# Kernel tuning notes

Hardware: AMD Instinct MI355X
Metric: run time of the kernel (lower is better)

The kernel has to match this reference:

```python
import jax, jax.numpy as jnp
import numpy as np

C_IN = 128
DIM = 2 * C_IN          # ELAN final channels = 2*in_channels = 256
WS = 8                  # window size
HEADS = 8
HEAD_DIM = DIM // HEADS
B, H, W = 4, 128, 128
LN_EPS = 1e-5


def setup_inputs() -> dict:
    key = jax.random.key(0)
    ks = jax.random.split(key, 20)
    mid = C_IN // 2  # middle_channels == block_channels == 64

    def p(k, shape, scale=0.05):
        return jax.random.normal(k, shape, jnp.float32) * scale

    return dict(
        x=jax.random.normal(ks[0], (B, C_IN, H, W), jnp.float32),
        # ELAN stem 1x1 convs: [main, short], each folded BN (scale, bias)
        w_stem=p(ks[1], (2, mid, C_IN, 1, 1)),
        s_stem=1.0 + p(ks[2], (2, mid)),
        b_stem=p(ks[3], (2, mid)),
        # 2 blocks x 2 convs of 3x3, mid->mid
        w_blk=p(ks[4], (4, mid, mid, 3, 3)),
        s_blk=1.0 + p(ks[5], (4, mid)),
        b_blk=p(ks[6], (4, mid)),
        # SwinV2 block params
        norm1_g=jnp.ones((DIM,), jnp.float32),
        norm1_b=jnp.zeros((DIM,), jnp.float32),
        qkv_w=p(ks[7], (3 * DIM, DIM)),
        qkv_b=p(ks[8], (3 * DIM,)).at[DIM:2 * DIM].set(0.0),  # V2 zeroes k bias
        proj_w=p(ks[9], (DIM, DIM)),
        proj_b=p(ks[10], (DIM,)),
        logit_scale=jnp.full((HEADS, 1, 1), float(np.log(10.0)), jnp.float32),
        cpb_w1=p(ks[11], (512, 2)),
        cpb_b1=p(ks[12], (512,)),
        cpb_w2=p(ks[13], (HEADS, 512)),
        norm2_g=jnp.ones((DIM,), jnp.float32),
        norm2_b=jnp.zeros((DIM,), jnp.float32),
        mlp_w1=p(ks[14], (DIM, DIM)),  # mlp_ratio=1.0
        mlp_b1=p(ks[15], (DIM,)),
        mlp_w2=p(ks[16], (DIM, DIM)),
        mlp_b2=p(ks[17], (DIM,)),
    )


def convbn(x, w, s, b, pad):
    # Conv(no bias) + eval-mode BN folded into per-channel scale/bias + SiLU
    y = jax.lax.conv_general_dilated(
        x, w, (1, 1), [(pad, pad), (pad, pad)],
        dimension_numbers=("NCHW", "OIHW", "NCHW"))
    y = y * s[None, :, None, None] + b[None, :, None, None]
    return jax.nn.silu(y)


def layernorm(x, g, b):
    m = jnp.mean(x, -1, keepdims=True)
    v = jnp.var(x, -1, keepdims=True)
    return (x - m) * jax.lax.rsqrt(v + LN_EPS) * g + b


def _rel_bias_consts():
    ws = WS
    ch = np.arange(-(ws - 1), ws, dtype=np.float32)
    table = np.stack(np.meshgrid(ch, ch, indexing="ij"), axis=-1)  # [2ws-1,2ws-1,2]
    table = table / (ws - 1) * 8.0
    table = np.sign(table) * np.log2(np.abs(table) + 1.0) / 3.0
    coords = np.stack(np.meshgrid(np.arange(ws), np.arange(ws), indexing="ij")).reshape(2, -1)
    rel = (coords[:, :, None] - coords[:, None, :]).transpose(1, 2, 0)  # [N,N,2]
    rel[..., 0] += ws - 1
    rel[..., 1] += ws - 1
    rel[..., 0] *= 2 * ws - 1
    idx = rel.sum(-1).reshape(-1)
    return jnp.asarray(table.reshape(-1, 2)), jnp.asarray(idx)


_TABLE, _IDX = _rel_bias_consts()


def elan_swin(x, w_stem, s_stem, b_stem, w_blk, s_blk, b_blk, norm1_g, norm1_b,
              qkv_w, qkv_b, proj_w, proj_b, logit_scale, cpb_w1, cpb_b1, cpb_w2,
              norm2_g, norm2_b, mlp_w1, mlp_b1, mlp_w2, mlp_b2):
    # ---- ELANBlock ----
    x_short = convbn(x, w_stem[1], s_stem[1], b_stem[1], 0)
    x_main = convbn(x, w_stem[0], s_stem[0], b_stem[0], 0)
    xb = x_main
    outs = []
    for i in range(2):
        xb = convbn(xb, w_blk[2 * i], s_blk[2 * i], b_blk[2 * i], 1)
        xb = convbn(xb, w_blk[2 * i + 1], s_blk[2 * i + 1], b_blk[2 * i + 1], 1)
        outs.append(xb)
    e = jnp.concatenate([outs[1], outs[0], x_main, x_short], axis=1)  # [B,DIM,H,W]
    e = e.transpose(0, 2, 3, 1)  # NHWC

    # ---- ShiftedWindowAttentionV2 (shift=0, H,W divisible by WS) ----
    Bn, Hh, Ww, Cc = e.shape
    nH, nW = Hh // WS, Ww // WS
    N = WS * WS
    xw = e.reshape(Bn, nH, WS, nW, WS, Cc).transpose(0, 1, 3, 2, 4, 5).reshape(-1, N, Cc)
    qkv = xw @ qkv_w.T + qkv_b
    qkv = qkv.reshape(-1, N, 3, HEADS, HEAD_DIM).transpose(2, 0, 3, 1, 4)
    q, k, v = qkv[0], qkv[1], qkv[2]  # [Bw, heads, N, d]
    qn = q / jnp.maximum(jnp.linalg.norm(q, axis=-1, keepdims=True), 1e-12)
    kn = k / jnp.maximum(jnp.linalg.norm(k, axis=-1, keepdims=True), 1e-12)
    attn = jnp.einsum("whnd,whmd->whnm", qn, kn)
    scale = jnp.exp(jnp.minimum(logit_scale, jnp.log(100.0)))  # [heads,1,1]
    attn = attn * scale[None]
    # continuous position bias MLP
    bias = jax.nn.relu(_TABLE @ cpb_w1.T + cpb_b1) @ cpb_w2.T  # [(2ws-1)^2, heads]
    bias = bias[_IDX].reshape(N, N, HEADS).transpose(2, 0, 1)
    bias = 16.0 * jax.nn.sigmoid(bias)
    attn = jax.nn.softmax(attn + bias[None], axis=-1)
    out = jnp.einsum("whnm,whmd->whnd", attn, v).transpose(0, 2, 1, 3).reshape(-1, N, Cc)
    out = out @ proj_w.T + proj_b
    out = out.reshape(Bn, nH, nW, WS, WS, Cc).transpose(0, 1, 3, 2, 4, 5).reshape(Bn, Hh, Ww, Cc)

    # ---- SwinTransformerBlockV2 (post-norm residuals) ----
    s = e + layernorm(out, norm1_g, norm1_b)
    h = s @ mlp_w1.T + mlp_b1
    h = jax.nn.gelu(h, approximate=False)
    h = h @ mlp_w2.T + mlp_b2
    s = s + layernorm(h, norm2_g, norm2_b)
    return s.transpose(0, 3, 1, 2)  # NCHW


def reference(x, w_stem, s_stem, b_stem, w_blk, s_blk, b_blk, norm1_g, norm1_b,
              qkv_w, qkv_b, proj_w, proj_b, logit_scale, cpb_w1, cpb_b1, cpb_w2,
              norm2_g, norm2_b, mlp_w1, mlp_b1, mlp_w2, mlp_b2):
    return elan_swin(x, w_stem, s_stem, b_stem, w_blk, s_blk, b_blk, norm1_g, norm1_b,
                     qkv_w, qkv_b, proj_w, proj_b, logit_scale, cpb_w1, cpb_b1, cpb_w2,
                     norm2_g, norm2_b, mlp_w1, mlp_b1, mlp_w2, mlp_b2)
```

## Files before the change

kernel.cpp:

```cpp
#include <hip/hip_runtime.h>
#include <hip/hip_bf16.h>
#include <math.h>


#define HW 16384
typedef unsigned int u32;
typedef unsigned short u16;
typedef __attribute__((ext_vector_type(8))) short short8;
typedef __attribute__((ext_vector_type(4))) float floatx4;

__device__ __forceinline__ float silu_f(float y) { return y / (1.f + expf(-y)); }
__device__ __forceinline__ float bflo(u32 u) { return __uint_as_float(u << 16); }
__device__ __forceinline__ float bfhi(u32 u) { return __uint_as_float(u & 0xffff0000u); }
__device__ __forceinline__ float bf2f(u16 v) { return __uint_as_float((u32)v << 16); }
__device__ __forceinline__ u16 f2bf(float x) {
  u32 u = __float_as_uint(x);
  u += 0x7fffu + ((u >> 16) & 1u);
  return (u16)(u >> 16);
}
__device__ __forceinline__ u32 pack2(float a, float b) {
  return (u32)f2bf(a) | ((u32)f2bf(b) << 16);
}

#define GLDS16(gp, lp)                                           \
  __builtin_amdgcn_global_load_lds(                              \
      (const __attribute__((address_space(1))) void*)(gp),       \
      (__attribute__((address_space(3))) void*)(lp), 16, 0, 0)

__global__ __launch_bounds__(256) void repack_kernel(
    const float* __restrict__ w_blk, const float* __restrict__ s_blk,
    const float* __restrict__ w_stem, const float* __restrict__ s_stem,
    u16* __restrict__ wtc, u16* __restrict__ wts) {
  int idx = blockIdx.x * 256 + threadIdx.x;
  if (idx < 147456) {
    int c = idx & 63;
    int rest = idx >> 6;
    int oc = rest & 63;
    int ct = rest >> 6;
    int conv = ct / 9, t = ct % 9;
    float w = w_blk[((size_t)(conv * 64 + oc) * 64 + c) * 9 + t];
    wtc[idx] = f2bf(w * s_blk[conv * 64 + oc]);
  } else if (idx < 147456 + 16384) {
    int j = idx - 147456;
    int c = j & 127, oc = j >> 7;
    float w = w_stem[(size_t)oc * 128 + c];
    wts[j] = f2bf(w * s_stem[oc]);
  }
}

__global__ __launch_bounds__(256) void castw_kernel(
    const float* __restrict__ in, u16* __restrict__ outp, int n) {
  int i = blockIdx.x * 256 + threadIdx.x;
  if (i < n) outp[i] = f2bf(in[i]);
}

__global__ __launch_bounds__(512) void cpb_mlp_kernel(
    const float* __restrict__ w1, const float* __restrict__ b1,
    const float* __restrict__ w2, float* __restrict__ pre) {
  __shared__ float hb[512];
  int t = blockIdx.x, j = threadIdx.x;
  int i = t / 15, jj = t % 15;
  float c0 = (float)(i - 7) * (8.f / 7.f);
  float c1 = (float)(jj - 7) * (8.f / 7.f);
  float s0 = (c0 > 0.f) ? 1.f : ((c0 < 0.f) ? -1.f : 0.f);
  float s1 = (c1 > 0.f) ? 1.f : ((c1 < 0.f) ? -1.f : 0.f);
  float t0 = s0 * log2f(fabsf(c0) + 1.f) * (1.f / 3.f);
  float t1 = s1 * log2f(fabsf(c1) + 1.f) * (1.f / 3.f);
  float h = t0 * w1[j * 2] + t1 * w1[j * 2 + 1] + b1[j];
  hb[j] = fmaxf(h, 0.f);
  __syncthreads();
  if (j < 8) {
    float s = 0.f;
    for (int k = 0; k < 512; ++k) s += hb[k] * w2[j * 512 + k];
    pre[t * 8 + j] = s;
  }
}

__global__ __launch_bounds__(256) void cpb_expand_kernel(
    const float* __restrict__ pre, float* __restrict__ bias_t) {
  int idx = blockIdx.x * 256 + threadIdx.x;
  int m = idx >> 6, n = idx & 63;
  int di = (n >> 3) - (m >> 3) + 7;
  int dj = (n & 7) - (m & 7) + 7;
  int ti = di * 15 + dj;
#pragma unroll
  for (int h = 0; h < 8; ++h) {
    float v = pre[ti * 8 + h];
    bias_t[h * 4096 + idx] = 16.f / (1.f + expf(-v));
  }
}

__global__ __launch_bounds__(256) void transpose_in_kernel(
    const float* __restrict__ x, u16* __restrict__ xt) {
  __shared__ float tl[64][65];
  int bid = blockIdx.x;
  int b = bid >> 9;
  int r = bid & 511;
  int cs = r >> 8, hws = r & 255;
  int c0 = cs << 6, hw0 = hws << 6;
  int tid = threadIdx.x;
  for (int e = tid; e < 4096; e += 256) {
    int c = e >> 6, p = e & 63;
    tl[c][p] = x[(size_t)(b * 128 + c0 + c) * HW + hw0 + p];
  }
  __syncthreads();
  for (int e = tid; e < 4096; e += 256) {
    int p = e >> 6, c = e & 63;
    xt[(size_t)(b * HW + hw0 + p) * 128 + c0 + c] = f2bf(tl[c][p]);
  }
}

__global__ __launch_bounds__(256, 4) void gemm_bf16_kernel(
    const u16* __restrict__ A, const u16* __restrict__ W,
    const float* __restrict__ bias, u16* __restrict__ C, int K, int ldc,
    int act) {
  __shared__ u16 As[128 * 64];
  __shared__ u16 Ws[64 * 64];
  int tid = threadIdx.x;
  int wv = tid >> 6, lane = tid & 63;
  int m0 = blockIdx.x * 128, n0 = blockIdx.y * 64;
  floatx4 zz = {0.f, 0.f, 0.f, 0.f};
  floatx4 acc[2][4];
#pragma unroll
  for (int i = 0; i < 2; ++i)
#pragma unroll
    for (int j = 0; j < 4; ++j) acc[i][j] = zz;
  int lr = lane >> 3, ls = lane & 7;
  for (int k0 = 0; k0 < K; k0 += 64) {
#pragma unroll
    for (int i = 0; i < 4; ++i) {
      int ci = wv * 4 + i;
      int r = ci * 8 + lr;
      int cc = ls ^ (r & 7);
      GLDS16(A + (size_t)(m0 + r) * K + k0 + cc * 8, As + ci * 512);
    }
#pragma unroll
    for (int i = 0; i < 2; ++i) {
      int ci = wv * 2 + i;
      int r = ci * 8 + lr;
      int cc = ls ^ (r & 7);
      GLDS16(W + (size_t)(n0 + r) * K + k0 + cc * 8, Ws + ci * 512);
    }
    __syncthreads();
#pragma unroll
    for (int kk = 0; kk < 2; ++kk) {
      int g = kk * 4 + (lane >> 4);
      short8 a0, a1, b0, b1, b2, b3;
      {
        int row = wv * 32 + (lane & 15);
        a0 = *(const short8*)&As[row * 64 + (g ^ (row & 7)) * 8];
        int row2 = row + 16;
        a1 = *(const short8*)&As[row2 * 64 + (g ^ (row2 & 7)) * 8];
      }
      {
        int col = lane & 15;
        b0 = *(const short8*)&Ws[col * 64 + (g ^ (col & 7)) * 8];
        int c1 = col + 16;
        b1 = *(const short8*)&Ws[c1 * 64 + (g ^ (c1 & 7)) * 8];
        int c2 = col + 32;
        b2 = *(const short8*)&Ws[c2 * 64 + (g ^ (c2 & 7)) * 8];
        int c3 = col + 48;
        b3 = *(const short8*)&Ws[c3 * 64 + (g ^ (c3 & 7)) * 8];
      }
      acc[0][0] = __builtin_amdgcn_mfma_f32_16x16x32_bf16(a0, b0, acc[0][0], 0, 0, 0);
      acc[0][1] = __builtin_amdgcn_mfma_f32_16x16x32_bf16(a0, b1, acc[0][1], 0, 0, 0);
      acc[0][2] = __builtin_amdgcn_mfma_f32_16x16x32_bf16(a0, b2, acc[0][2], 0, 0, 0);
      acc[0][3] = __builtin_amdgcn_mfma_f32_16x16x32_bf16(a0, b3, acc[0][3], 0, 0, 0);
      acc[1][0] = __builtin_amdgcn_mfma_f32_16x16x32_bf16(a1, b0, acc[1][0], 0, 0, 0);
      acc[1][1] = __builtin_amdgcn_mfma_f32_16x16x32_bf16(a1, b1, acc[1][1], 0, 0, 0);
      acc[1][2] = __builtin_amdgcn_mfma_f32_16x16x32_bf16(a1, b2, acc[1][2], 0, 0, 0);
      acc[1][3] = __builtin_amdgcn_mfma_f32_16x16x32_bf16(a1, b3, acc[1][3], 0, 0, 0);
    }
    __syncthreads();
  }
  int rbase = wv * 32 + ((lane >> 4) << 2);
  int cb = lane & 15;
#pragma unroll
  for (int mi = 0; mi < 2; ++mi) {
#pragma unroll
    for (int nj = 0; nj < 4; ++nj) {
      int col = n0 + nj * 16 + cb;
      float bv = bias[col];
#pragma unroll
      for (int r = 0; r < 4; ++r) {
        int row = m0 + rbase + mi * 16 + r;
        float v = acc[mi][nj][r] + bv;
        if (act == 1) v = 0.5f * v * (1.f + erff(v * 0.70710678118654752f));
        else if (act == 2) v = silu_f(v);
        C[(size_t)row * ldc + col] = f2bf(v);
      }
    }
  }
}

__global__ __launch_bounds__(256) void conv3x3_mfma_kernel(
    const u16* __restrict__ in, int istr, u16* __restrict__ outp, int ostr,
    const u16* __restrict__ wt, const float* __restrict__ bias) {
  __shared__ u16 tile[6400];
  int tid = threadIdx.x;
  int wv = tid >> 6, lane = tid & 63;
  int bx = blockIdx.x, by = blockIdx.y, b = blockIdx.z;
  int h0 = by * 8, w0 = bx * 8;
#pragma unroll
  for (int rr = 0; rr < 4; ++rr) {
    int slot = rr * 256 + tid;
    int p = slot >> 3, ch = slot & 7;
    if (p < 100) {
      int hr = p / 10, hc = p % 10;
      int gh = h0 + hr - 1, gw = w0 + hc - 1;
      bool ok = (gh >= 0) && (gh < 128) && (gw >= 0) && (gw < 128);
      uint4 v = {0u, 0u, 0u, 0u};
      if (ok) {
        size_t pix = (size_t)((b * 128 + gh) * 128 + gw);
        v = *(const uint4*)(in + pix * istr + ch * 8);
      }
      *(uint4*)(tile + p * 64 + ((ch ^ (p & 7)) << 3)) = v;
    }
  }
  __syncthreads();
  int pl = lane & 15;
  int g = lane >> 4;
  int prow = 2 * wv + (pl >> 3), pcol = pl & 7;
  floatx4 zz = {0.f, 0.f, 0.f, 0.f};
  floatx4 acc[4] = {zz, zz, zz, zz};
#pragma unroll
  for (int t = 0; t < 9; ++t) {
    int dy = t / 3, dx = t % 3;
    int hp = (prow + dy) * 10 + (pcol + dx);
    short8 bf0 = *(const short8*)&tile[hp * 64 + (((0 * 4 + g) ^ (hp & 7)) << 3)];
    short8 bf1 = *(const short8*)&tile[hp * 64 + (((1 * 4 + g) ^ (hp & 7)) << 3)];
    const u16* wtap = wt + t * 4096;
#pragma unroll
    for (int nf = 0; nf < 4; ++nf) {
      short8 a0 = *(const short8*)&wtap[(nf * 16 + pl) * 64 + g * 8];
      short8 a1 = *(const short8*)&wtap[(nf * 16 + pl) * 64 + 32 + g * 8];
      acc[nf] = __builtin_amdgcn_mfma_f32_16x16x32_bf16(a0, bf0, acc[nf], 0, 0, 0);
      acc[nf] = __builtin_amdgcn_mfma_f32_16x16x32_bf16(a1, bf1, acc[nf], 0, 0, 0);
    }
  }
  size_t pix = (size_t)((b * 128 + h0 + prow) * 128 + w0 + pcol);
#pragma unroll
  for (int nf = 0; nf < 4; ++nf) {
    float o0 = silu_f(acc[nf][0] + bias[nf * 16 + g * 4 + 0]);
    float o1 = silu_f(acc[nf][1] + bias[nf * 16 + g * 4 + 1]);
    float o2 = silu_f(acc[nf][2] + bias[nf * 16 + g * 4 + 2]);
    float o3 = silu_f(acc[nf][3] + bias[nf * 16 + g * 4 + 3]);
    uint2 w2;
    w2.x = pack2(o0, o1);
    w2.y = pack2(o2, o3);
    *(uint2*)(outp + pix * ostr + nf * 16 + g * 4) = w2;
  }
}

__global__ __launch_bounds__(256) void attn_mfma_kernel(
    const u16* __restrict__ qkv, const float* __restrict__ logit_scale,
    const float* __restrict__ bias_t, u16* __restrict__ ao) {
  __shared__ __align__(16) char lds[4 * 10240 + 4 * 4608];
  int tid = threadIdx.x;
  int w = tid >> 6, l = tid & 63;
  int wid = blockIdx.x >> 1;
  int h = __builtin_amdgcn_readfirstlane(((blockIdx.x & 1) << 2) + w);
  char* Aq = lds + w * 10240;
  char* Ak = Aq + 5120;
  char* Pt = Aq;
  char* Vt = lds + 40960 + w * 4608;
  char* Ol = Vt;

  int b = wid >> 8, wh = (wid >> 4) & 15, ww = wid & 15;
  int p = (b << 14) + ((wh * 8 + (l >> 3)) << 7) + ww * 8 + (l & 7);
  const u32* qp = (const u32*)(qkv + (size_t)p * 768 + h * 32);
  float scale = __expf(fminf(logit_scale[h], 4.6051701860f));
  int lc = l & 15, lg = l >> 4;

  {
    float f[32];
    float s = 0.f;
#pragma unroll
    for (int i = 0; i < 16; ++i) {
      u32 u = qp[i];
      f[2 * i] = bflo(u);
      f[2 * i + 1] = bfhi(u);
    }
#pragma unroll
    for (int d = 0; d < 32; ++d) s += f[d] * f[d];
    float r = scale / fmaxf(sqrtf(s), 1e-12f);
    uint4* dst = (uint4*)(Aq + l * 80);
#pragma unroll
    for (int c = 0; c < 4; ++c) {
      uint4 v;
      v.x = pack2(f[c * 8 + 0] * r, f[c * 8 + 1] * r);
      v.y = pack2(f[c * 8 + 2] * r, f[c * 8 + 3] * r);
      v.z = pack2(f[c * 8 + 4] * r, f[c * 8 + 5] * r);
      v.w = pack2(f[c * 8 + 6] * r, f[c * 8 + 7] * r);
      dst[c] = v;
    }
  }
  {
    float f[32];
    float s = 0.f;
#pragma unroll
    for (int i = 0; i < 16; ++i) {
      u32 u = qp[128 + i];
      f[2 * i] = bflo(u);
      f[2 * i + 1] = bfhi(u);
    }
#pragma unroll
    for (int d = 0; d < 32; ++d) s += f[d] * f[d];
    float r = 1.f / fmaxf(sqrtf(s), 1e-12f);
    uint4* dst = (uint4*)(Ak + l * 80);
#pragma unroll
    for (int c = 0; c < 4; ++c) {
      uint4 v;
      v.x = pack2(f[c * 8 + 0] * r, f[c * 8 + 1] * r);
      v.y = pack2(f[c * 8 + 2] * r, f[c * 8 + 3] * r);
      v.z = pack2(f[c * 8 + 4] * r, f[c * 8 + 5] * r);
      v.w = pack2(f[c * 8 + 6] * r, f[c * 8 + 7] * r);
      dst[c] = v;
    }
  }
  {
#pragma unroll
    for (int i = 0; i < 16; ++i) {
      u32 u = qp[256 + i];
      *(u16*)(Vt + (2 * i) * 144 + l * 2) = (u16)(u & 0xffffu);
      *(u16*)(Vt + (2 * i + 1) * 144 + l * 2) = (u16)(u >> 16);
    }
  }

  short8 kf[4], qf[4];
#pragma unroll
  for (int i = 0; i < 4; ++i) {
    kf[i] = *(const short8*)(Ak + (i * 16 + lc) * 80 + (lg << 4));
    qf[i] = *(const short8*)(Aq + (i * 16 + lc) * 80 + (lg << 4));
  }
  floatx4 zz = {0.f, 0.f, 0.f, 0.f};
  floatx4 S[4][4];
#pragma unroll
  for (int mi = 0; mi < 4; ++mi)
#pragma unroll
    for (int ni = 0; ni < 4; ++ni) S[mi][ni] = zz;
#pragma unroll
  for (int mi = 0; mi < 4; ++mi)
#pragma unroll
    for (int ni = 0; ni < 4; ++ni)
      S[mi][ni] = __builtin_amdgcn_mfma_f32_16x16x32_bf16(kf[mi], qf[ni], S[mi][ni], 0, 0, 0);

  const float* bh = bias_t + h * 4096;
  float den[4] = {0.f, 0.f, 0.f, 0.f};
#pragma unroll
  for (int mi = 0; mi < 4; ++mi) {
    int mb = mi * 16 + (lg << 2);
#pragma unroll
    for (int ni = 0; ni < 4; ++ni) {
      int nn = ni * 16 + lc;
#pragma unroll
      for (int r = 0; r < 4; ++r) {
        float e = __expf(S[mi][ni][r] + bh[(mb + r) * 64 + nn]);
        S[mi][ni][r] = e;
        den[ni] += e;
      }
    }
  }
#pragma unroll
  for (int ni = 0; ni < 4; ++ni) {
    den[ni] += __shfl_xor(den[ni], 16);
    den[ni] += __shfl_xor(den[ni], 32);
    den[ni] = 1.f / den[ni];
  }

#pragma unroll
  for (int ni = 0; ni < 4; ++ni)
#pragma unroll
    for (int mi = 0; mi < 4; ++mi) {
      uint2 v;
      v.x = pack2(S[mi][ni][0] * den[ni], S[mi][ni][1] * den[ni]);
      v.y = pack2(S[mi][ni][2] * den[ni], S[mi][ni][3] * den[ni]);
      *(uint2*)(Pt + (ni * 16 + lc) * 144 + mi * 32 + (lg << 3)) = v;
    }

  short8 vf[2][2];
#pragma unroll
  for (int ks = 0; ks < 2; ++ks)
#pragma unroll
    for (int db = 0; db < 2; ++db)
      vf[ks][db] = *(const short8*)(Vt + (db * 16 + lc) * 144 + ks * 64 + (lg << 4));
  floatx4 O[4][2];
#pragma unroll
  for (int nb = 0; nb < 4; ++nb) {
    O[nb][0] = zz;
    O[nb][1] = zz;
  }
#pragma unroll
  for (int nb = 0; nb < 4; ++nb) {
    short8 pf0 = *(const short8*)(Pt + (nb * 16 + lc) * 144 + (lg << 4));
    short8 pf1 = *(const short8*)(Pt + (nb * 16 + lc) * 144 + 64 + (lg << 4));
    O[nb][0] = __builtin_amdgcn_mfma_f32_16x16x32_bf16(pf0, vf[0][0], O[nb][0], 0, 0, 0);
    O[nb][0] = __builtin_amdgcn_mfma_f32_16x16x32_bf16(pf1, vf[1][0], O[nb][0], 0, 0, 0);
    O[nb][1] = __builtin_amdgcn_mfma_f32_16x16x32_bf16(pf0, vf[0][1], O[nb][1], 0, 0, 0);
    O[nb][1] = __builtin_amdgcn_mfma_f32_16x16x32_bf16(pf1, vf[1][1], O[nb][1], 0, 0, 0);
  }

#pragma unroll
  for (int nb = 0; nb < 4; ++nb)
#pragma unroll
    for (int r = 0; r < 4; ++r) {
      int n = nb * 16 + (lg << 2) + r;
      *(u16*)(Ol + n * 72 + lc * 2) = f2bf(O[nb][0][r]);
      *(u16*)(Ol + n * 72 + (16 + lc) * 2) = f2bf(O[nb][1][r]);
    }
  u32 ov[16];
#pragma unroll
  for (int j = 0; j < 16; ++j) ov[j] = *(const u32*)(Ol + l * 72 + j * 4);
  uint4* op = (uint4*)(ao + (size_t)(wid * 64 + l) * 256 + h * 32);
#pragma unroll
  for (int q4 = 0; q4 < 4; ++q4) {
    uint4 v;
    v.x = ov[q4 * 4 + 0];
    v.y = ov[q4 * 4 + 1];
    v.z = ov[q4 * 4 + 2];
    v.w = ov[q4 * 4 + 3];
    op[q4] = v;
  }
}

__global__ __launch_bounds__(256) void ln1v_kernel(
    const u16* __restrict__ pin, const u16* __restrict__ ebf,
    u16* __restrict__ sbf, const float* __restrict__ g,
    const float* __restrict__ bb) {
  int tid = threadIdx.x;
  int bid = blockIdx.x;
  int b = bid >> 8, hw0 = (bid & 255) << 6;
  int i = tid >> 2, qq = tid & 3;
  int hw = hw0 + i;
  int him = hw >> 7, wim = hw & 127;
  int wid = b * 256 + (him >> 3) * 16 + (wim >> 3);
  int t = wid * 64 + (him & 7) * 8 + (wim & 7);
  size_t pbase = (size_t)t * 256 + qq * 64;
  size_t ebase = ((size_t)(b * HW + hw)) * 256 + qq * 64;
  float v[64];
  float s1 = 0.f, s2 = 0.f;
#pragma unroll
  for (int j = 0; j < 8; ++j) {
    uint4 u = *(const uint4*)(pin + pbase + j * 8);
    u32 ua[4] = {u.x, u.y, u.z, u.w};
#pragma unroll
    for (int k = 0; k < 4; ++k) {
      float a = bflo(ua[k]), c = bfhi(ua[k]);
      v[j * 8 + 2 * k] = a;
      v[j * 8 + 2 * k + 1] = c;
      s1 += a + c;
      s2 += a * a + c * c;
    }
  }
  s1 += __shfl_xor(s1, 1);
  s1 += __shfl_xor(s1, 2);
  s2 += __shfl_xor(s2, 1);
  s2 += __shfl_xor(s2, 2);
  float mean = s1 * (1.f / 256.f);
  float var = s2 * (1.f / 256.f) - mean * mean;
  float rs = rsqrtf(var + 1e-5f);
#pragma unroll
  for (int j = 0; j < 8; ++j) {
    uint4 u = *(const uint4*)(ebf + ebase + j * 8);
    u32 ua[4] = {u.x, u.y, u.z, u.w};
    uint4 o;
    u32 ow[4];
#pragma unroll
    for (int k = 0; k < 4; ++k) {
      int c = qq * 64 + j * 8 + 2 * k;
      float o0 = bflo(ua[k]) + (v[j * 8 + 2 * k] - mean) * rs * g[c] + bb[c];
      float o1 = bfhi(ua[k]) + (v[j * 8 + 2 * k + 1] - mean) * rs * g[c + 1] + bb[c + 1];
      ow[k] = pack2(o0, o1);
    }
    o.x = ow[0]; o.y = ow[1]; o.z = ow[2]; o.w = ow[3];
    *(uint4*)(sbf + ebase + j * 8) = o;
  }
}

__global__ __launch_bounds__(256) void ln2t_kernel(
    const u16* __restrict__ h2, const u16* __restrict__ sbf,
    const float* __restrict__ g, const float* __restrict__ bb,
    float* __restrict__ outp) {
  __shared__ float tile[64][257];
  int tid = threadIdx.x;
  int bid = blockIdx.x;
  int b = bid >> 8, hw0 = (bid & 255) << 6;
  int i = tid >> 2, qq = tid & 3;
  size_t base = ((size_t)(b * HW + hw0 + i)) * 256 + qq * 64;
  float v[64];
  float s1 = 0.f, s2 = 0.f;
#pragma unroll
  for (int j = 0; j < 8; ++j) {
    uint4 u = *(const uint4*)(h2 + base + j * 8);
    u32 ua[4] = {u.x, u.y, u.z, u.w};
#pragma unroll
    for (int k = 0; k < 4; ++k) {
      float a = bflo(ua[k]), c = bfhi(ua[k]);
      v[j * 8 + 2 * k] = a;
      v[j * 8 + 2 * k + 1] = c;
      s1 += a + c;
      s2 += a * a + c * c;
    }
  }
  s1 += __shfl_xor(s1, 1);
  s1 += __shfl_xor(s1, 2);
  s2 += __shfl_xor(s2, 1);
  s2 += __shfl_xor(s2, 2);
  float mean = s1 * (1.f / 256.f);
  float var = s2 * (1.f / 256.f) - mean * mean;
  float rs = rsqrtf(var + 1e-5f);
#pragma unroll
  for (int j = 0; j < 8; ++j) {
    uint4 u = *(const uint4*)(sbf + base + j * 8);
    u32 ua[4] = {u.x, u.y, u.z, u.w};
#pragma unroll
    for (int k = 0; k < 4; ++k) {
      int c = qq * 64 + j * 8 + 2 * k;
      tile[i][c] = bflo(ua[k]) + (v[j * 8 + 2 * k] - mean) * rs * g[c] + bb[c];
      tile[i][c + 1] = bfhi(ua[k]) + (v[j * 8 + 2 * k + 1] - mean) * rs * g[c + 1] + bb[c + 1];
    }
  }
  __syncthreads();
  int pl = tid & 63, cq = tid >> 6;
#pragma unroll 8
  for (int cc = 0; cc < 64; ++cc) {
    int c = cq * 64 + cc;
    outp[((size_t)(b * 256 + c)) * HW + hw0 + pl] = tile[pl][c];
  }
}

extern "C" void kernel_launch(void* const* d_in, const int* in_sizes, int n_in,
                              void* d_out, int out_size, void* d_ws, size_t ws_size,
                              hipStream_t stream) {
  const float* x        = (const float*)d_in[0];
  const float* w_stem   = (const float*)d_in[1];
  const float* s_stem   = (const float*)d_in[2];
  const float* b_stem   = (const float*)d_in[3];
  const float* w_blk    = (const float*)d_in[4];
  const float* s_blk    = (const float*)d_in[5];
  const float* b_blk    = (const float*)d_in[6];
  const float* norm1_g  = (const float*)d_in[7];
  const float* norm1_b  = (const float*)d_in[8];
  const float* qkv_w    = (const float*)d_in[9];
  const float* qkv_b    = (const float*)d_in[10];
  const float* proj_w   = (const float*)d_in[11];
  const float* proj_b   = (const float*)d_in[12];
  const float* logit_sc = (const float*)d_in[13];
  const float* cpb_w1   = (const float*)d_in[14];
  const float* cpb_b1   = (const float*)d_in[15];
  const float* cpb_w2   = (const float*)d_in[16];
  const float* norm2_g  = (const float*)d_in[17];
  const float* norm2_b  = (const float*)d_in[18];
  const float* mlp_w1   = (const float*)d_in[19];
  const float* mlp_b1   = (const float*)d_in[20];
  const float* mlp_w2   = (const float*)d_in[21];
  const float* mlp_b2   = (const float*)d_in[22];
  float* out = (float*)d_out;
  float* ws = (float*)d_ws;
  (void)in_sizes; (void)n_in; (void)out_size; (void)ws_size;

  float* R0 = ws;
  float* R1 = ws + 16777216;
  float* R2 = ws + 33554432;
  float* TAIL = ws + 50331648;
  u16* WTC  = (u16*)TAIL;
  u16* WTS  = (u16*)(TAIL + 73728);
  u16* QWB  = (u16*)(TAIL + 81920);
  u16* PWB  = (u16*)(TAIL + 180224);
  u16* M1WB = (u16*)(TAIL + 212992);
  u16* M2WB = (u16*)(TAIL + 245760);
  float* BPRE = TAIL + 278528;
  float* BFT  = TAIL + 280576;

  u16* XT  = (u16*)R2;
  u16* EBF = (u16*)(R2 + 8388608);
  u16* T1  = (u16*)R1;
  u16* T2  = (u16*)(R1 + 2097152);
  u16* QKV = (u16*)R1;
  u16* AO  = (u16*)R0;
  u16* P   = (u16*)(R0 + 8388608);
  u16* SBF = (u16*)R0;
  u16* Hb  = (u16*)R2;
  u16* H2  = (u16*)(R0 + 8388608);

  repack_kernel<<<640, 256, 0, stream>>>(w_blk, s_blk, w_stem, s_stem, WTC, WTS);
  castw_kernel<<<768, 256, 0, stream>>>(qkv_w, QWB, 196608);
  castw_kernel<<<256, 256, 0, stream>>>(proj_w, PWB, 65536);
  castw_kernel<<<256, 256, 0, stream>>>(mlp_w1, M1WB, 65536);
  castw_kernel<<<256, 256, 0, stream>>>(mlp_w2, M2WB, 65536);
  cpb_mlp_kernel<<<225, 512, 0, stream>>>(cpb_w1, cpb_b1, cpb_w2, BPRE);
  cpb_expand_kernel<<<16, 256, 0, stream>>>(BPRE, BFT);

  transpose_in_kernel<<<2048, 256, 0, stream>>>(x, XT);
  dim3 gs(512, 2);
  gemm_bf16_kernel<<<gs, 256, 0, stream>>>(XT, WTS, b_stem, EBF + 128, 128, 256, 2);

  dim3 cgrid(16, 16, 4);
  conv3x3_mfma_kernel<<<cgrid, 256, 0, stream>>>(EBF + 128, 256, T1, 64, WTC, b_blk);
  conv3x3_mfma_kernel<<<cgrid, 256, 0, stream>>>(T1, 64, EBF + 64, 256, WTC + 9 * 4096, b_blk + 64);
  conv3x3_mfma_kernel<<<cgrid, 256, 0, stream>>>(EBF + 64, 256, T2, 64, WTC + 18 * 4096, b_blk + 128);
  conv3x3_mfma_kernel<<<cgrid, 256, 0, stream>>>(T2, 64, EBF, 256, WTC + 27 * 4096, b_blk + 192);

  dim3 gq(512, 12);
  gemm_bf16_kernel<<<gq, 256, 0, stream>>>(EBF, QWB, qkv_b, QKV, 256, 768, 0);

  attn_mfma_kernel<<<2048, 256, 0, stream>>>(QKV, logit_sc, BFT, AO);

  dim3 g4(512, 4);
  gemm_bf16_kernel<<<g4, 256, 0, stream>>>(AO, PWB, proj_b, P, 256, 256, 0);
  ln1v_kernel<<<1024, 256, 0, stream>>>(P, EBF, SBF, norm1_g, norm1_b);
  gemm_bf16_kernel<<<g4, 256, 0, stream>>>(SBF, M1WB, mlp_b1, Hb, 256, 256, 1);
  gemm_bf16_kernel<<<g4, 256, 0, stream>>>(Hb, M2WB, mlp_b2, H2, 256, 256, 0);
  ln2t_kernel<<<1024, 256, 0, stream>>>(H2, SBF, norm2_g, norm2_b, out);
}
```

Measured before the change: 464.3 us.

## Fuse QKV projection into window attention kernel with split-bf16 QK products

Removes the separate QKV GEMM and its 768-channel intermediate buffer. Each attention block now loads the 64-pixel window of the embedding into LDS and computes its four heads' Q, K and V with MFMA, reading the weights straight from global memory. The normalized Q and K are split into hi and lo bf16 parts, and the attention scores use three MFMAs for extra precision. Costs include redundant weight reads per block, triple MFMA work for the scores, and higher LDS use (72KB per block), which may lower occupancy.

```diff
diff --git a/kernel.cpp b/kernel.cpp
--- a/kernel.cpp
+++ b/kernel.cpp
@@ -8,6 +8,8 @@
 typedef unsigned short u16;
 typedef __attribute__((ext_vector_type(8))) short short8;
 typedef __attribute__((ext_vector_type(4))) float floatx4;
+
+#define MEMBAR() asm volatile("" ::: "memory")
 
 __device__ __forceinline__ float silu_f(float y) { return y / (1.f + expf(-y)); }
 __device__ __forceinline__ float bflo(u32 u) { return __uint_as_float(u << 16); }
@@ -252,98 +254,175 @@
   }
 }
 
-__global__ __launch_bounds__(256) void attn_mfma_kernel(
-    const u16* __restrict__ qkv, const float* __restrict__ logit_scale,
+__device__ __forceinline__ void qkv_mm(const u16* Elds, const u16* qwb,
+                                       int moff, int h, int lc, int lg,
+                                       floatx4 acc[4][2]) {
+  floatx4 zz = {0.f, 0.f, 0.f, 0.f};
+#pragma unroll
+  for (int mf = 0; mf < 4; ++mf) {
+    acc[mf][0] = zz;
+    acc[mf][1] = zz;
+  }
+#pragma unroll
+  for (int ks = 0; ks < 8; ++ks) {
+    int ch = ks >> 1, g = ((ks & 1) << 2) + lg;
+    short8 af[4];
+#pragma unroll
+    for (int mf = 0; mf < 4; ++mf) {
+      int tk = mf * 16 + lc;
+      af[mf] = *(const short8*)&Elds[(ch * 64 + tk) * 64 + ((g ^ (tk & 7)) << 3)];
+    }
+#pragma unroll
+    for (int nf = 0; nf < 2; ++nf) {
+      short8 bf = *(const short8*)(qwb +
+          (size_t)(moff + h * 32 + nf * 16 + lc) * 256 + ks * 32 + lg * 8);
+#pragma unroll
+      for (int mf = 0; mf < 4; ++mf)
+        acc[mf][nf] =
+            __builtin_amdgcn_mfma_f32_16x16x32_bf16(af[mf], bf, acc[mf][nf], 0, 0, 0);
+    }
+  }
+}
+
+__global__ __launch_bounds__(256) void attn_fused_kernel(
+    const u16* __restrict__ ebf, const u16* __restrict__ qwb,
+    const float* __restrict__ qkv_b, const float* __restrict__ logit_scale,
     const float* __restrict__ bias_t, u16* __restrict__ ao) {
-  __shared__ __align__(16) char lds[4 * 10240 + 4 * 4608];
+  __shared__ __align__(16) char lds[73728];
   int tid = threadIdx.x;
   int w = tid >> 6, l = tid & 63;
   int wid = blockIdx.x >> 1;
   int h = __builtin_amdgcn_readfirstlane(((blockIdx.x & 1) << 2) + w);
-  char* Aq = lds + w * 10240;
-  char* Ak = Aq + 5120;
-  char* Pt = Aq;
-  char* Vt = lds + 40960 + w * 4608;
+  u16* Elds = (u16*)lds;
+  char* Kn = lds + 32768 + w * 10240;
+  char* Qn = Kn + 5120;
+  char* Pt = Kn;
+  char* Vt = lds + w * 4608;
   char* Ol = Vt;
 
   int b = wid >> 8, wh = (wid >> 4) & 15, ww = wid & 15;
-  int p = (b << 14) + ((wh * 8 + (l >> 3)) << 7) + ww * 8 + (l & 7);
-  const u32* qp = (const u32*)(qkv + (size_t)p * 768 + h * 32);
+  int pixbase = (b << 14) + wh * 1024 + ww * 8;
+  {
+    int lr = l >> 3, ls = l & 7;
+#pragma unroll
+    for (int j = 0; j < 8; ++j) {
+      int pix = pixbase + j * 128 + lr;
+      GLDS16(ebf + (size_t)pix * 256 + w * 64 + ((ls ^ lr) << 3),
+             Elds + (w * 8 + j) * 512);
+    }
+  }
+  __syncthreads();
+
+  int lc = l & 15, lg = l >> 4;
   float scale = __expf(fminf(logit_scale[h], 4.6051701860f));
-  int lc = l & 15, lg = l >> 4;
-
+  floatx4 macc[4][2];
+  float rnrm[4][4];
+  short8 kf_hi[4], kf_lo[4], qf_hi[4], qf_lo[4];
+
+  qkv_mm(Elds, qwb, 256, h, lc, lg, macc);
+#pragma unroll
+  for (int mf = 0; mf < 4; ++mf)
+#pragma unroll
+    for (int r = 0; r < 4; ++r) {
+      float v0 = macc[mf][0][r], v1 = macc[mf][1][r];
+      float ss = v0 * v0 + v1 * v1;
+      ss += __shfl_xor(ss, 1);
+      ss += __shfl_xor(ss, 2);
+      ss += __shfl_xor(ss, 4);
+      ss += __shfl_xor(ss, 8);
+      float rk = 1.f / fmaxf(sqrtf(ss), 1e-12f);
+      rnrm[mf][r] = rk;
+      int tk = mf * 16 + (lg << 2) + r;
+      *(u16*)(Kn + tk * 80 + lc * 2) = f2bf(v0 * rk);
+      *(u16*)(Kn + tk * 80 + (16 + lc) * 2) = f2bf(v1 * rk);
+    }
+  MEMBAR();
+#pragma unroll
+  for (int i = 0; i < 4; ++i)
+    kf_hi[i] = *(const short8*)(Kn + (i * 16 + lc) * 80 + (lg << 4));
+  MEMBAR();
+#pragma unroll
+  for (int mf = 0; mf < 4; ++mf)
+#pragma unroll
+    for (int r = 0; r < 4; ++r) {
+      int tk = mf * 16 + (lg << 2) + r;
+      float s0 = macc[mf][0][r] * rnrm[mf][r];
+      float s1 = macc[mf][1][r] * rnrm[mf][r];
+      *(u16*)(Kn + tk * 80 + lc * 2) = f2bf(s0 - bf2f(f2bf(s0)));
+      *(u16*)(Kn + tk * 80 + (16 + lc) * 2) = f2bf(s1 - bf2f(f2bf(s1)));
+    }
+  MEMBAR();
+#pragma unroll
+  for (int i = 0; i < 4; ++i)
+    kf_lo[i] = *(const short8*)(Kn + (i * 16 + lc) * 80 + (lg << 4));
+  MEMBAR();
+
+  qkv_mm(Elds, qwb, 0, h, lc, lg, macc);
   {
-    float f[32];
-    float s = 0.f;
-#pragma unroll
-    for (int i = 0; i < 16; ++i) {
-      u32 u = qp[i];
-      f[2 * i] = bflo(u);
-      f[2 * i + 1] = bfhi(u);
-    }
-#pragma unroll
-    for (int d = 0; d < 32; ++d) s += f[d] * f[d];
-    float r = scale / fmaxf(sqrtf(s), 1e-12f);
-    uint4* dst = (uint4*)(Aq + l * 80);
-#pragma unroll
-    for (int c = 0; c < 4; ++c) {
-      uint4 v;
-      v.x = pack2(f[c * 8 + 0] * r, f[c * 8 + 1] * r);
-      v.y = pack2(f[c * 8 + 2] * r, f[c * 8 + 3] * r);
-      v.z = pack2(f[c * 8 + 4] * r, f[c * 8 + 5] * r);
-      v.w = pack2(f[c * 8 + 6] * r, f[c * 8 + 7] * r);
-      dst[c] = v;
-    }
-  }
-  {
-    float f[32];
-    float s = 0.f;
-#pragma unroll
-    for (int i = 0; i < 16; ++i) {
-      u32 u = qp[128 + i];
-      f[2 * i] = bflo(u);
-      f[2 * i + 1] = bfhi(u);
-    }
-#pragma unroll
-    for (int d = 0; d < 32; ++d) s += f[d] * f[d];
-    float r = 1.f / fmaxf(sqrtf(s), 1e-12f);
-    uint4* dst = (uint4*)(Ak + l * 80);
-#pragma unroll
-    for (int c = 0; c < 4; ++c) {
-      uint4 v;
-      v.x = pack2(f[c * 8 + 0] * r, f[c * 8 + 1] * r);
-      v.y = pack2(f[c * 8 + 2] * r, f[c * 8 + 3] * r);
-      v.z = pack2(f[c * 8 + 4] * r, f[c * 8 + 5] * r);
-      v.w = pack2(f[c * 8 + 6] * r, f[c * 8 + 7] * r);
-      dst[c] = v;
-    }
-  }
-  {
-#pragma unroll
-    for (int i = 0; i < 16; ++i) {
-      u32 u = qp[256 + i];
-      *(u16*)(Vt + (2 * i) * 144 + l * 2) = (u16)(u & 0xffffu);
-      *(u16*)(Vt + (2 * i + 1) * 144 + l * 2) = (u16)(u >> 16);
-    }
-  }
-
-  short8 kf[4], qf[4];
-#pragma unroll
-  for (int i = 0; i < 4; ++i) {
-    kf[i] = *(const short8*)(Ak + (i * 16 + lc) * 80 + (lg << 4));
-    qf[i] = *(const short8*)(Aq + (i * 16 + lc) * 80 + (lg << 4));
-  }
+    float qb0 = qkv_b[h * 32 + lc], qb1 = qkv_b[h * 32 + 16 + lc];
+#pragma unroll
+    for (int mf = 0; mf < 4; ++mf)
+#pragma unroll
+      for (int r = 0; r < 4; ++r) {
+        float v0 = macc[mf][0][r] + qb0, v1 = macc[mf][1][r] + qb1;
+        macc[mf][0][r] = v0;
+        macc[mf][1][r] = v1;
+        float ss = v0 * v0 + v1 * v1;
+        ss += __shfl_xor(ss, 1);
+        ss += __shfl_xor(ss, 2);
+        ss += __shfl_xor(ss, 4);
+        ss += __shfl_xor(ss, 8);
+        float rq = scale / fmaxf(sqrtf(ss), 1e-12f);
+        rnrm[mf][r] = rq;
+        int tk = mf * 16 + (lg << 2) + r;
+        *(u16*)(Qn + tk * 80 + lc * 2) = f2bf(v0 * rq);
+        *(u16*)(Qn + tk * 80 + (16 + lc) * 2) = f2bf(v1 * rq);
+      }
+    MEMBAR();
+#pragma unroll
+    for (int i = 0; i < 4; ++i)
+      qf_hi[i] = *(const short8*)(Qn + (i * 16 + lc) * 80 + (lg << 4));
+    MEMBAR();
+#pragma unroll
+    for (int mf = 0; mf < 4; ++mf)
+#pragma unroll
+      for (int r = 0; r < 4; ++r) {
+        int tk = mf * 16 + (lg << 2) + r;
+        float s0 = macc[mf][0][r] * rnrm[mf][r];
+        float s1 = macc[mf][1][r] * rnrm[mf][r];
+        *(u16*)(Qn + tk * 80 + lc * 2) = f2bf(s0 - bf2f(f2bf(s0)));
+        *(u16*)(Qn + tk * 80 + (16 + lc) * 2) = f2bf(s1 - bf2f(f2bf(s1)));
+      }
+    MEMBAR();
+#pragma unroll
+    for (int i = 0; i < 4; ++i)
+      qf_lo[i] = *(const short8*)(Qn + (i * 16 + lc) * 80 + (lg << 4));
+    MEMBAR();
+  }
+
+  qkv_mm(Elds, qwb, 512, h, lc, lg, macc);
+  float vb0 = qkv_b[512 + h * 32 + lc], vb1 = qkv_b[512 + h * 32 + 16 + lc];
+  __syncthreads();
+#pragma unroll
+  for (int mf = 0; mf < 4; ++mf)
+#pragma unroll
+    for (int r = 0; r < 4; ++r) {
+      int tk = mf * 16 + (lg << 2) + r;
+      *(u16*)(Vt + lc * 144 + tk * 2) = f2bf(macc[mf][0][r] + vb0);
+      *(u16*)(Vt + (16 + lc) * 144 + tk * 2) = f2bf(macc[mf][1][r] + vb1);
+    }
+  MEMBAR();
+
   floatx4 zz = {0.f, 0.f, 0.f, 0.f};
   floatx4 S[4][4];
 #pragma unroll
   for (int mi = 0; mi < 4; ++mi)
 #pragma unroll
-    for (int ni = 0; ni < 4; ++ni) S[mi][ni] = zz;
-#pragma unroll
-  for (int mi = 0; mi < 4; ++mi)
-#pragma unroll
-    for (int ni = 0; ni < 4; ++ni)
-      S[mi][ni] = __builtin_amdgcn_mfma_f32_16x16x32_bf16(kf[mi], qf[ni], S[mi][ni], 0, 0, 0);
+    for (int ni = 0; ni < 4; ++ni) {
+      floatx4 a = __builtin_amdgcn_mfma_f32_16x16x32_bf16(kf_lo[mi], qf_hi[ni], zz, 0, 0, 0);
+      a = __builtin_amdgcn_mfma_f32_16x16x32_bf16(kf_hi[mi], qf_lo[ni], a, 0, 0, 0);
+      S[mi][ni] = __builtin_amdgcn_mfma_f32_16x16x32_bf16(kf_hi[mi], qf_hi[ni], a, 0, 0, 0);
+    }
 
   const float* bh = bias_t + h * 4096;
   float den[4] = {0.f, 0.f, 0.f, 0.f};
@@ -367,7 +446,6 @@
     den[ni] += __shfl_xor(den[ni], 32);
     den[ni] = 1.f / den[ni];
   }
-
 #pragma unroll
   for (int ni = 0; ni < 4; ++ni)
 #pragma unroll
@@ -377,7 +455,7 @@
       v.y = pack2(S[mi][ni][2] * den[ni], S[mi][ni][3] * den[ni]);
       *(uint2*)(Pt + (ni * 16 + lc) * 144 + mi * 32 + (lg << 3)) = v;
     }
-
+  MEMBAR();
   short8 vf[2][2];
 #pragma unroll
   for (int ks = 0; ks < 2; ++ks)
@@ -399,7 +477,7 @@
     O[nb][1] = __builtin_amdgcn_mfma_f32_16x16x32_bf16(pf0, vf[0][1], O[nb][1], 0, 0, 0);
     O[nb][1] = __builtin_amdgcn_mfma_f32_16x16x32_bf16(pf1, vf[1][1], O[nb][1], 0, 0, 0);
   }
-
+  MEMBAR();
 #pragma unroll
   for (int nb = 0; nb < 4; ++nb)
 #pragma unroll
@@ -408,6 +486,7 @@
       *(u16*)(Ol + n * 72 + lc * 2) = f2bf(O[nb][0][r]);
       *(u16*)(Ol + n * 72 + (16 + lc) * 2) = f2bf(O[nb][1][r]);
     }
+  MEMBAR();
   u32 ov[16];
 #pragma unroll
   for (int j = 0; j < 16; ++j) ov[j] = *(const u32*)(Ol + l * 72 + j * 4);
@@ -576,7 +655,6 @@
   u16* EBF = (u16*)(R2 + 8388608);
   u16* T1  = (u16*)R1;
   u16* T2  = (u16*)(R1 + 2097152);
-  u16* QKV = (u16*)R1;
   u16* AO  = (u16*)R0;
   u16* P   = (u16*)(R0 + 8388608);
   u16* SBF = (u16*)R0;
@@ -601,10 +679,7 @@
   conv3x3_mfma_kernel<<<cgrid, 256, 0, stream>>>(EBF + 64, 256, T2, 64, WTC + 18 * 4096, b_blk + 128);
   conv3x3_mfma_kernel<<<cgrid, 256, 0, stream>>>(T2, 64, EBF, 256, WTC + 27 * 4096, b_blk + 192);
 
-  dim3 gq(512, 12);
-  gemm_bf16_kernel<<<gq, 256, 0, stream>>>(EBF, QWB, qkv_b, QKV, 256, 768, 0);
-
-  attn_mfma_kernel<<<2048, 256, 0, stream>>>(QKV, logit_sc, BFT, AO);
+  attn_fused_kernel<<<2048, 256, 0, stream>>>(EBF, QWB, qkv_b, logit_sc, BFT, AO);
 
   dim3 g4(512, 4);
   gemm_bf16_kernel<<<g4, 256, 0, stream>>>(AO, PWB, proj_b, P, 256, 256, 0);
```

New measurement: 443.2 us. -4.6%, faster.
